# Kernel optimization log

Measured on AMD Instinct MI355X. Metric: run time of the kernel, lower is better.

The kernel has to match this reference:

```python
import jax, jax.numpy as jnp
import numpy as np


def _unfold(x, k):
    # x: [B, C, H, W] -> [B, C, S, L] with S=k*k (row-major patch order), L=H*W
    B, C, H, W = x.shape
    pad = k // 2
    xp = jnp.pad(x, ((0, 0), (0, 0), (pad, pad), (pad, pad)))
    patches = jnp.stack(
        [xp[:, :, r:r + H, c:c + W] for r in range(k) for c in range(k)], axis=2
    )  # [B, C, S, H, W]
    return patches.reshape(B, C, k * k, H * W)


def setup_inputs() -> dict:
    key = jax.random.key(0)
    ks = jax.random.split(key, 8)
    B, C, H, W = 8, 64, 128, 128
    R, Cout = 4, 128
    x = jax.random.normal(ks[0], (B, C, H, W), dtype=jnp.float32)
    gate_w = jax.random.normal(ks[1], (R, C), dtype=jnp.float32) * 0.05   # 1x1 gate conv weight
    gate_b = jax.random.normal(ks[2], (R,), dtype=jnp.float32) * 0.01
    theta = jax.random.normal(ks[3], (R,), dtype=jnp.float32) * 0.5       # learned directions
    raw_sigma_u = jax.random.normal(ks[4], (R,), dtype=jnp.float32) * 0.1
    raw_sigma_s = jax.random.normal(ks[5], (R,), dtype=jnp.float32) * 0.1
    pw_w = jax.random.normal(ks[6], (Cout, R * C), dtype=jnp.float32) * (1.0 / np.sqrt(R * C).astype(np.float32))
    pw_b = jax.random.normal(ks[7], (Cout,), dtype=jnp.float32) * 0.01
    return {"x": x, "gate_w": gate_w, "gate_b": gate_b, "theta": theta,
            "raw_sigma_u": raw_sigma_u, "raw_sigma_s": raw_sigma_s,
            "pw_w": pw_w, "pw_b": pw_b}


def reference(x, gate_w, gate_b, theta, raw_sigma_u, raw_sigma_s, pw_w, pw_b):
    k = 3
    B, C, H, W = x.shape
    R = theta.shape[0]
    S, L = k * k, H * W

    x_un = _unfold(x, k)                                         # [B, C, S, L]

    # 1x1 gate conv + fuzzy softmax over rules
    logits = jnp.einsum('bchw,rc->brhw', x, gate_w) + gate_b[None, :, None, None]
    mu = jax.nn.softmax(logits, axis=1)                          # [B, R, H, W]
    mu_un = _unfold(mu, k)                                       # [B, R, S, L]
    s_center = (k // 2) * k + (k // 2)
    mu_center = mu_un[:, :, s_center:s_center + 1, :]            # [B, R, 1, L]

    # anisotropic Gaussian kernel per rule over integer offsets (row-major)
    grid = np.arange(k, dtype=np.float32) - k // 2
    dy = jnp.asarray(np.repeat(grid, k))                         # [S]
    dx = jnp.asarray(np.tile(grid, k))                           # [S]
    cos_t, sin_t = jnp.cos(theta)[:, None], jnp.sin(theta)[:, None]
    proj_u = cos_t * dx[None, :] + sin_t * dy[None, :]           # [R, S]
    proj_s = -sin_t * dx[None, :] + cos_t * dy[None, :]
    su = (jax.nn.softplus(raw_sigma_u) + 1e-4)[:, None]
    ss = (jax.nn.softplus(raw_sigma_s) + 1e-4)[:, None]
    kern = jnp.exp(-proj_u ** 2 / su ** 2 - proj_s ** 2 / ss ** 2)  # [R, S]

    alpha = mu_center * mu_un * kern[None, :, :, None]           # [B, R, S, L]
    alpha_sum = jnp.maximum(alpha.sum(axis=(1, 2), keepdims=True), 1e-8)
    alpha = alpha / alpha_sum

    agg = jnp.einsum('brsl,bcsl->brcl', alpha, x_un)             # [B, R, C, L]
    agg_flat = agg.reshape(B, R * C, L)
    out = jnp.einsum('bnl,on->bol', agg_flat, pw_w) + pw_b[None, :, None]
    return out.reshape(B, -1, H, W)
```

## Files before the change

### kernel.cpp

```cpp
#include <hip/hip_runtime.h>
#include <math.h>

#define CC 64
#define RR 4
#define HH 128
#define WW 128
#define BB 8
#define COUT 128
#define XCH 164

typedef __attribute__((ext_vector_type(8))) short short8;
typedef __attribute__((ext_vector_type(4))) float f32x4;
typedef __attribute__((ext_vector_type(2))) float f32x2;

__device__ __forceinline__ unsigned short f2bf(float f) {
  unsigned u = __float_as_uint(f);
  u += 0x7fffu + ((u >> 16) & 1u);
  return (unsigned short)(u >> 16);
}
__device__ __forceinline__ float bf2f(unsigned short h) {
  return __uint_as_float(((unsigned)h) << 16);
}

__global__ __launch_bounds__(256) void k_pre(const float* __restrict__ theta,
                                             const float* __restrict__ rsu,
                                             const float* __restrict__ rss,
                                             const float* __restrict__ pw,
                                             float* __restrict__ wkern,
                                             unsigned short* __restrict__ pwb) {
  int i = blockIdx.x * 256 + threadIdx.x;
  if (i < COUT * RR * CC) pwb[i] = f2bf(pw[i]);
  if (blockIdx.x == 0 && threadIdx.x < RR * 9) {
    int t = threadIdx.x;
    int r = t / 9, s = t % 9;
    float dy = (float)(s / 3 - 1), dx = (float)(s % 3 - 1);
    float ct = cosf(theta[r]), st = sinf(theta[r]);
    float su = log1pf(expf(rsu[r])) + 1e-4f;
    float sv = log1pf(expf(rss[r])) + 1e-4f;
    float pu = ct * dx + st * dy;
    float ps = -st * dx + ct * dy;
    wkern[t] = expf(-(pu * pu) / (su * su) - (ps * ps) / (sv * sv));
  }
}

__global__ __launch_bounds__(256, 3) void k_fused(const float* __restrict__ x,
                                                  const float* __restrict__ gw,
                                                  const float* __restrict__ gb,
                                                  const float* __restrict__ wkern,
                                                  const unsigned short* __restrict__ pwb,
                                                  const float* __restrict__ pb,
                                                  float* __restrict__ out) {
  __shared__ unsigned short xs[CC][XCH];
  __shared__ float mus[RR][4][40];
  __shared__ float alp[36][64];
  __shared__ float rsum[RR][64];
  __shared__ unsigned short aggs[32][264];

  int tid = threadIdx.x;
  int raw = blockIdx.x;
  int bid = (raw & 7) * 256 + (raw >> 3);
  int b = bid >> 8;
  int rem = bid & 255;
  int h0 = (rem >> 2) << 1;
  int w0 = (rem & 3) << 5;

  {
    int c4 = tid & 15;
    int pr0 = tid >> 4;
    if (c4 < 10) {
      int gcol = w0 - 4 + (c4 << 2);
      bool colok = (unsigned)gcol < WW;
      #pragma unroll
      for (int k = 0; k < 16; ++k) {
        int pair = (k << 4) + pr0;
        int c = pair >> 2, row = pair & 3;
        int grow = h0 - 1 + row;
        float4 v = make_float4(0.f, 0.f, 0.f, 0.f);
        if (colok && (unsigned)grow < HH)
          v = *(const float4*)(x + (((size_t)b * CC + c) << 14) + (grow << 7) + gcol);
        ushort4 uv;
        uv.x = f2bf(v.x); uv.y = f2bf(v.y); uv.z = f2bf(v.z); uv.w = f2bf(v.w);
        *(ushort4*)&xs[c][row * 40 + (c4 << 2)] = uv;
      }
    }
  }
  __syncthreads();

  if (tid < 136) {
    int y = tid / 34, cxo = tid % 34;
    int cx = 3 + cxo;
    int grow = h0 - 1 + y, gcol = w0 - 1 + cxo;
    float lg0 = gb[0], lg1 = gb[1], lg2 = gb[2], lg3 = gb[3];
    #pragma unroll 8
    for (int c = 0; c < CC; ++c) {
      float xv = bf2f(xs[c][y * 40 + cx]);
      lg0 = fmaf(xv, gw[c], lg0);
      lg1 = fmaf(xv, gw[64 + c], lg1);
      lg2 = fmaf(xv, gw[128 + c], lg2);
      lg3 = fmaf(xv, gw[192 + c], lg3);
    }
    float m = fmaxf(fmaxf(lg0, lg1), fmaxf(lg2, lg3));
    float e0 = expf(lg0 - m), e1 = expf(lg1 - m);
    float e2 = expf(lg2 - m), e3 = expf(lg3 - m);
    float inv = 1.0f / (e0 + e1 + e2 + e3);
    if (!((unsigned)grow < HH && (unsigned)gcol < WW)) inv = 0.0f;
    mus[0][y][cx] = e0 * inv;
    mus[1][y][cx] = e1 * inv;
    mus[2][y][cx] = e2 * inv;
    mus[3][y][cx] = e3 * inv;
  }
  __syncthreads();

  {
    int t = tid & 63, r = tid >> 6;
    int prow = t >> 5, pcol = t & 31;
    float mc = mus[r][prow + 1][pcol + 4];
    float sum = 0.f;
    #pragma unroll
    for (int s = 0; s < 9; ++s) {
      int sr = s / 3, sc = s % 3;
      float a = mc * mus[r][prow + sr][pcol + 3 + sc] * wkern[r * 9 + s];
      alp[r * 9 + s][t] = a;
      sum += a;
    }
    rsum[r][t] = sum;
  }

  int lane = tid & 63;
  int wv = tid >> 6;
  int lr = lane & 15, lq = lane >> 4;
  int o0 = wv << 5;

  short8 a0r[8], a1r[8];
  {
    const unsigned short* pA = pwb + ((o0 + lr) << 8) + (lq << 3);
    #pragma unroll
    for (int ks = 0; ks < 8; ++ks) {
      a0r[ks] = *(const short8*)(pA + (ks << 5));
      a1r[ks] = *(const short8*)(pA + 4096 + (ks << 5));
    }
  }
  __syncthreads();

  #pragma unroll
  for (int p = 0; p < 2; ++p) {
    {
      int t = tid & 31, cg = tid >> 5, c0 = cg << 3;
      int px = (p << 5) + t;
      float inv = 1.0f / fmaxf(rsum[0][px] + rsum[1][px] + rsum[2][px] + rsum[3][px], 1e-8f);
      f32x2 cacc[4][4];
      #pragma unroll
      for (int r = 0; r < 4; ++r)
        #pragma unroll
        for (int j = 0; j < 4; ++j) cacc[r][j] = (f32x2){0.f, 0.f};

      #pragma unroll
      for (int s = 0; s < 9; ++s) {
        int sr = s / 3, sc = s % 3;
        int xo = (p + sr) * 40 + t + 3 + sc;
        f32x2 xv[4];
        #pragma unroll
        for (int j = 0; j < 4; ++j) {
          xv[j][0] = bf2f(xs[c0 + 2 * j][xo]);
          xv[j][1] = bf2f(xs[c0 + 2 * j + 1][xo]);
        }
        #pragma unroll
        for (int r = 0; r < 4; ++r) {
          float av = alp[r * 9 + s][px];
          f32x2 av2 = {av, av};
          #pragma unroll
          for (int j = 0; j < 4; ++j) cacc[r][j] += av2 * xv[j];
        }
      }
      #pragma unroll
      for (int r = 0; r < 4; ++r) {
        short8 wvv;
        #pragma unroll
        for (int j = 0; j < 4; ++j) {
          wvv[2 * j]     = (short)f2bf(cacc[r][j][0] * inv);
          wvv[2 * j + 1] = (short)f2bf(cacc[r][j][1] * inv);
        }
        *(short8*)&aggs[t][(r << 6) + c0] = wvv;
      }
    }
    __syncthreads();

    f32x4 dacc[2][2];
    #pragma unroll
    for (int i = 0; i < 2; ++i)
      #pragma unroll
      for (int j = 0; j < 2; ++j) dacc[i][j] = (f32x4){0.f, 0.f, 0.f, 0.f};

    #pragma unroll
    for (int ks = 0; ks < 8; ++ks) {
      short8 b0 = *(const short8*)&aggs[lr][(ks << 5) + (lq << 3)];
      short8 b1 = *(const short8*)&aggs[16 + lr][(ks << 5) + (lq << 3)];
      dacc[0][0] = __builtin_amdgcn_mfma_f32_16x16x32_bf16(a0r[ks], b0, dacc[0][0], 0, 0, 0);
      dacc[0][1] = __builtin_amdgcn_mfma_f32_16x16x32_bf16(a0r[ks], b1, dacc[0][1], 0, 0, 0);
      dacc[1][0] = __builtin_amdgcn_mfma_f32_16x16x32_bf16(a1r[ks], b0, dacc[1][0], 0, 0, 0);
      dacc[1][1] = __builtin_amdgcn_mfma_f32_16x16x32_bf16(a1r[ks], b1, dacc[1][1], 0, 0, 0);
    }

    #pragma unroll
    for (int oi = 0; oi < 2; ++oi) {
      #pragma unroll
      for (int q = 0; q < 4; ++q) {
        int o = o0 + (oi << 4) + (lq << 2) + q;
        float bias = pb[o];
        size_t base = (((size_t)b * COUT + o) << 14) + ((h0 + p) << 7) + w0;
        out[base + lr]      = dacc[oi][0][q] + bias;
        out[base + 16 + lr] = dacc[oi][1][q] + bias;
      }
    }
    if (p == 0) __syncthreads();
  }
}

extern "C" void kernel_launch(void* const* d_in, const int* in_sizes, int n_in,
                              void* d_out, int out_size, void* d_ws, size_t ws_size,
                              hipStream_t stream) {
  const float* x     = (const float*)d_in[0];
  const float* gw    = (const float*)d_in[1];
  const float* gb    = (const float*)d_in[2];
  const float* theta = (const float*)d_in[3];
  const float* rsu   = (const float*)d_in[4];
  const float* rss   = (const float*)d_in[5];
  const float* pw    = (const float*)d_in[6];
  const float* pb    = (const float*)d_in[7];
  float* outp = (float*)d_out;

  float* wkern = (float*)d_ws;
  unsigned short* pwb = (unsigned short*)(wkern + 64);

  k_pre<<<128, 256, 0, stream>>>(theta, rsu, rss, pw, wkern, pwb);
  k_fused<<<BB * (HH / 2) * (WW / 32), 256, 0, stream>>>(x, gw, gb, wkern, pwb, pb, outp);
}
```

Before: 60.27 us.

## Store alpha as packed bf16, compute Gaussian kernel in-block, prefetch weights early

Alpha weights are now stored in shared memory as bf16, laid out per pixel with the 4 rules adjacent. Each thread loads all 9 taps' alphas as uint2 up front, which cuts LDS reads in the aggregation loop. The x tap loads are double-buffered one tap ahead. The Gaussian kernel is now computed inside every block, so the wkern workspace and the small k_pre branch go away. The MFMA weight fragments and the bias are loaded before the x staging, and the gate loop unroll is raised. In exchange, alpha loses precision to bf16, the transcendental math is repeated in every block, and the early weight loads raise register pressure.

```diff
diff --git a/kernel.cpp b/kernel.cpp
--- a/kernel.cpp
+++ b/kernel.cpp
@@ -8,6 +8,7 @@
 #define BB 8
 #define COUT 128
 #define XCH 164
+#define ALS 44
 
 typedef __attribute__((ext_vector_type(8))) short short8;
 typedef __attribute__((ext_vector_type(4))) float f32x4;
@@ -22,39 +23,26 @@
   return __uint_as_float(((unsigned)h) << 16);
 }
 
-__global__ __launch_bounds__(256) void k_pre(const float* __restrict__ theta,
-                                             const float* __restrict__ rsu,
-                                             const float* __restrict__ rss,
-                                             const float* __restrict__ pw,
-                                             float* __restrict__ wkern,
+__global__ __launch_bounds__(256) void k_pre(const float* __restrict__ pw,
                                              unsigned short* __restrict__ pwb) {
   int i = blockIdx.x * 256 + threadIdx.x;
-  if (i < COUT * RR * CC) pwb[i] = f2bf(pw[i]);
-  if (blockIdx.x == 0 && threadIdx.x < RR * 9) {
-    int t = threadIdx.x;
-    int r = t / 9, s = t % 9;
-    float dy = (float)(s / 3 - 1), dx = (float)(s % 3 - 1);
-    float ct = cosf(theta[r]), st = sinf(theta[r]);
-    float su = log1pf(expf(rsu[r])) + 1e-4f;
-    float sv = log1pf(expf(rss[r])) + 1e-4f;
-    float pu = ct * dx + st * dy;
-    float ps = -st * dx + ct * dy;
-    wkern[t] = expf(-(pu * pu) / (su * su) - (ps * ps) / (sv * sv));
-  }
+  pwb[i] = f2bf(pw[i]);
 }
 
 __global__ __launch_bounds__(256, 3) void k_fused(const float* __restrict__ x,
                                                   const float* __restrict__ gw,
                                                   const float* __restrict__ gb,
-                                                  const float* __restrict__ wkern,
+                                                  const float* __restrict__ theta,
+                                                  const float* __restrict__ rsu,
+                                                  const float* __restrict__ rss,
                                                   const unsigned short* __restrict__ pwb,
                                                   const float* __restrict__ pb,
                                                   float* __restrict__ out) {
   __shared__ unsigned short xs[CC][XCH];
   __shared__ float mus[RR][4][40];
-  __shared__ float alp[36][64];
+  __shared__ unsigned short alp[64][ALS];
   __shared__ float rsum[RR][64];
-  __shared__ unsigned short aggs[32][264];
+  __shared__ __align__(16) unsigned short aggs[32][264];
 
   int tid = threadIdx.x;
   int raw = blockIdx.x;
@@ -63,6 +51,23 @@
   int rem = bid & 255;
   int h0 = (rem >> 2) << 1;
   int w0 = (rem & 3) << 5;
+
+  int lane = tid & 63;
+  int wv = tid >> 6;
+  int lr = lane & 15, lq = lane >> 4;
+  int o0 = wv << 5;
+
+  short8 a0r[8], a1r[8];
+  {
+    const unsigned short* pA = pwb + ((o0 + lr) << 8) + (lq << 3);
+    #pragma unroll
+    for (int ks = 0; ks < 8; ++ks) {
+      a0r[ks] = *(const short8*)(pA + (ks << 5));
+      a1r[ks] = *(const short8*)(pA + 4096 + (ks << 5));
+    }
+  }
+  float4 pbv0 = *(const float4*)&pb[o0 + (lq << 2)];
+  float4 pbv1 = *(const float4*)&pb[o0 + 16 + (lq << 2)];
 
   {
     int c4 = tid & 15;
@@ -91,7 +96,7 @@
     int cx = 3 + cxo;
     int grow = h0 - 1 + y, gcol = w0 - 1 + cxo;
     float lg0 = gb[0], lg1 = gb[1], lg2 = gb[2], lg3 = gb[3];
-    #pragma unroll 8
+    #pragma unroll 16
     for (int c = 0; c < CC; ++c) {
       float xv = bf2f(xs[c][y * 40 + cx]);
       lg0 = fmaf(xv, gw[c], lg0);
@@ -113,32 +118,25 @@
 
   {
     int t = tid & 63, r = tid >> 6;
+    float th = theta[r];
+    float ct = cosf(th), st = sinf(th);
+    float su = log1pf(expf(rsu[r])) + 1e-4f;
+    float sv = log1pf(expf(rss[r])) + 1e-4f;
+    float isu = 1.0f / (su * su), isv = 1.0f / (sv * sv);
     int prow = t >> 5, pcol = t & 31;
     float mc = mus[r][prow + 1][pcol + 4];
     float sum = 0.f;
     #pragma unroll
     for (int s = 0; s < 9; ++s) {
-      int sr = s / 3, sc = s % 3;
-      float a = mc * mus[r][prow + sr][pcol + 3 + sc] * wkern[r * 9 + s];
-      alp[r * 9 + s][t] = a;
-      sum += a;
+      float dy = (float)(s / 3 - 1), dx = (float)(s % 3 - 1);
+      float pu = ct * dx + st * dy;
+      float ps = -st * dx + ct * dy;
+      float kern = expf(-pu * pu * isu - ps * ps * isv);
+      float av = mc * mus[r][prow + s / 3][pcol + 3 + s % 3] * kern;
+      alp[t][(s << 2) + r] = f2bf(av);
+      sum += av;
     }
     rsum[r][t] = sum;
-  }
-
-  int lane = tid & 63;
-  int wv = tid >> 6;
-  int lr = lane & 15, lq = lane >> 4;
-  int o0 = wv << 5;
-
-  short8 a0r[8], a1r[8];
-  {
-    const unsigned short* pA = pwb + ((o0 + lr) << 8) + (lq << 3);
-    #pragma unroll
-    for (int ks = 0; ks < 8; ++ks) {
-      a0r[ks] = *(const short8*)(pA + (ks << 5));
-      a1r[ks] = *(const short8*)(pA + 4096 + (ks << 5));
-    }
   }
   __syncthreads();
 
@@ -148,28 +146,50 @@
       int t = tid & 31, cg = tid >> 5, c0 = cg << 3;
       int px = (p << 5) + t;
       float inv = 1.0f / fmaxf(rsum[0][px] + rsum[1][px] + rsum[2][px] + rsum[3][px], 1e-8f);
+
+      uint2 ad[9];
+      #pragma unroll
+      for (int s = 0; s < 9; ++s) ad[s] = *(const uint2*)(&alp[px][s << 2]);
+
       f32x2 cacc[4][4];
       #pragma unroll
       for (int r = 0; r < 4; ++r)
         #pragma unroll
         for (int j = 0; j < 4; ++j) cacc[r][j] = (f32x2){0.f, 0.f};
 
+      f32x2 xv[2][4];
+      {
+        int xo = p * 40 + t + 3;
+        #pragma unroll
+        for (int j = 0; j < 4; ++j) {
+          xv[0][j][0] = bf2f(xs[c0 + 2 * j][xo]);
+          xv[0][j][1] = bf2f(xs[c0 + 2 * j + 1][xo]);
+        }
+      }
       #pragma unroll
       for (int s = 0; s < 9; ++s) {
-        int sr = s / 3, sc = s % 3;
-        int xo = (p + sr) * 40 + t + 3 + sc;
-        f32x2 xv[4];
+        if (s < 8) {
+          int sn = s + 1;
+          int xo = (p + sn / 3) * 40 + t + 3 + sn % 3;
+          #pragma unroll
+          for (int j = 0; j < 4; ++j) {
+            xv[(s + 1) & 1][j][0] = bf2f(xs[c0 + 2 * j][xo]);
+            xv[(s + 1) & 1][j][1] = bf2f(xs[c0 + 2 * j + 1][xo]);
+          }
+        }
+        unsigned adx = ad[s].x, ady = ad[s].y;
+        float af0 = __uint_as_float(adx << 16);
+        float af1 = __uint_as_float(adx & 0xffff0000u);
+        float af2 = __uint_as_float(ady << 16);
+        float af3 = __uint_as_float(ady & 0xffff0000u);
+        f32x2 A0 = {af0, af0}, A1 = {af1, af1}, A2 = {af2, af2}, A3 = {af3, af3};
         #pragma unroll
         for (int j = 0; j < 4; ++j) {
-          xv[j][0] = bf2f(xs[c0 + 2 * j][xo]);
-          xv[j][1] = bf2f(xs[c0 + 2 * j + 1][xo]);
-        }
-        #pragma unroll
-        for (int r = 0; r < 4; ++r) {
-          float av = alp[r * 9 + s][px];
-          f32x2 av2 = {av, av};
-          #pragma unroll
-          for (int j = 0; j < 4; ++j) cacc[r][j] += av2 * xv[j];
+          f32x2 xvj = xv[s & 1][j];
+          cacc[0][j] += A0 * xvj;
+          cacc[1][j] += A1 * xvj;
+          cacc[2][j] += A2 * xvj;
+          cacc[3][j] += A3 * xvj;
         }
       }
       #pragma unroll
@@ -203,13 +223,13 @@
 
     #pragma unroll
     for (int oi = 0; oi < 2; ++oi) {
+      float4 pbv = oi ? pbv1 : pbv0;
       #pragma unroll
       for (int q = 0; q < 4; ++q) {
         int o = o0 + (oi << 4) + (lq << 2) + q;
-        float bias = pb[o];
         size_t base = (((size_t)b * COUT + o) << 14) + ((h0 + p) << 7) + w0;
-        out[base + lr]      = dacc[oi][0][q] + bias;
-        out[base + 16 + lr] = dacc[oi][1][q] + bias;
+        out[base + lr]      = dacc[oi][0][q] + pbv[q];
+        out[base + 16 + lr] = dacc[oi][1][q] + pbv[q];
       }
     }
     if (p == 0) __syncthreads();
@@ -229,9 +249,9 @@
   const float* pb    = (const float*)d_in[7];
   float* outp = (float*)d_out;
 
-  float* wkern = (float*)d_ws;
-  unsigned short* pwb = (unsigned short*)(wkern + 64);
-
-  k_pre<<<128, 256, 0, stream>>>(theta, rsu, rss, pw, wkern, pwb);
-  k_fused<<<BB * (HH / 2) * (WW / 32), 256, 0, stream>>>(x, gw, gb, wkern, pwb, pb, outp);
-}
+  unsigned short* pwb = (unsigned short*)d_ws;
+
+  k_pre<<<(COUT * RR * CC) / 256, 256, 0, stream>>>(pw, pwb);
+  k_fused<<<BB * (HH / 2) * (WW / 32), 256, 0, stream>>>(x, gw, gb, theta, rsu, rss,
+                                                         pwb, pb, outp);
+}
```

After: 68.74 us. +14.0%, slower.
